# Performance work log

Hardware: AMD Instinct MI355X
Metric: run time of the kernel (lower is better)

The kernel has to match this reference:

```python
import jax, jax.numpy as jnp
import numpy as np

DIM = 1024
NUM_HEADS = 16
HEAD_DIM = DIM // NUM_HEADS


def apply_rope(x):
    # x: [B, S, H, D]
    seq_len = x.shape[1]
    inv_freq = 1.0 / (10000.0 ** (jnp.arange(0, HEAD_DIM, 2, dtype=jnp.float32) / HEAD_DIM))
    t = jnp.arange(seq_len, dtype=jnp.float32)
    freqs = jnp.outer(t, inv_freq)                      # [S, D/2]
    emb = jnp.concatenate([freqs, freqs], axis=-1)      # [S, D]
    cos = jnp.cos(emb)[None, :, None, :]                # [1, S, 1, D]
    sin = jnp.sin(emb)[None, :, None, :]
    x1, x2 = jnp.split(x, 2, axis=-1)
    x_rot = jnp.concatenate([-x2, x1], axis=-1)
    return x * cos + x_rot * sin


def setup_inputs() -> dict:
    key = jax.random.key(0)
    kx, kq, kk, kv, ko = jax.random.split(key, 5)
    scale = 1.0 / np.sqrt(DIM)
    return {
        "x": jax.random.normal(kx, (2, 2048, DIM), dtype=jnp.float32),
        "Wq": jax.random.normal(kq, (DIM, DIM), dtype=jnp.float32) * scale,
        "Wk": jax.random.normal(kk, (DIM, DIM), dtype=jnp.float32) * scale,
        "Wv": jax.random.normal(kv, (DIM, DIM), dtype=jnp.float32) * scale,
        "Wo": jax.random.normal(ko, (DIM, DIM), dtype=jnp.float32) * scale,
    }


def reference(x, Wq, Wk, Wv, Wo):
    B, S, _ = x.shape
    # torch nn.Linear: y = x @ W.T
    q = (x @ Wq.T).reshape(B, S, NUM_HEADS, HEAD_DIM)
    k = (x @ Wk.T).reshape(B, S, NUM_HEADS, HEAD_DIM)
    v = (x @ Wv.T).reshape(B, S, NUM_HEADS, HEAD_DIM)
    q = apply_rope(q)
    k = apply_rope(k)
    # attention over [B, H, S, D]; non-causal, no dropout (eval mode)
    scale = 1.0 / np.sqrt(HEAD_DIM)
    scores = jnp.einsum("bqhd,bkhd->bhqk", q, k) * scale
    attn = jax.nn.softmax(scores, axis=-1)
    out = jnp.einsum("bhqk,bkhd->bqhd", attn, v).reshape(B, S, DIM)
    return out @ Wo.T
```

## Files before the change

### kernel.cpp

```cpp
#include <hip/hip_runtime.h>

#define DIM   1024
#define NHEAD 16
#define HD    64
#define SEQ   2048
#define BATCH 2
#define MROWS (BATCH * SEQ)
#define NT    (SEQ / 64)

typedef __attribute__((ext_vector_type(8))) _Float16 s8h;
typedef __attribute__((ext_vector_type(4))) _Float16 s4h;
typedef __attribute__((ext_vector_type(4))) float f32x4;

typedef const __attribute__((address_space(1))) unsigned GU;
typedef __attribute__((address_space(3))) unsigned LU;

__device__ __forceinline__ void gll16(const void* g, void* l) {
    __builtin_amdgcn_global_load_lds((GU*)g, (LU*)l, 16, 0, 0);
}
__device__ __forceinline__ f32x4 mfma16(s8h a, s8h b, f32x4 c) {
    return __builtin_amdgcn_mfma_f32_16x16x32_f16(a, b, c, 0, 0, 0);
}
__device__ __forceinline__ float ex2(float x) {
    return __builtin_amdgcn_exp2f(x);
}

__global__ __launch_bounds__(256) void cast_f16_kernel(
    const float* __restrict__ x,  const float* __restrict__ wq,
    const float* __restrict__ wk, const float* __restrict__ wv,
    const float* __restrict__ wo,
    _Float16* __restrict__ xh,  _Float16* __restrict__ wqh,
    _Float16* __restrict__ wkh, _Float16* __restrict__ wvh,
    _Float16* __restrict__ woh) {
    int id = blockIdx.x * 256 + threadIdx.x;
    const float* src; _Float16* dst; size_t off;
    if (id < 524288) { src = x; dst = xh; off = (size_t)id * 8; }
    else {
        int r = id - 524288, w = r >> 17, o = r & 131071;
        src = (w == 0) ? wq : (w == 1) ? wk : (w == 2) ? wv : wo;
        dst = (w == 0) ? wqh : (w == 1) ? wkh : (w == 2) ? wvh : woh;
        off = (size_t)o * 8;
    }
    float4 v0 = *(const float4*)(src + off);
    float4 v1 = *(const float4*)(src + off + 4);
    s8h y;
    y[0]=(_Float16)v0.x; y[1]=(_Float16)v0.y; y[2]=(_Float16)v0.z; y[3]=(_Float16)v0.w;
    y[4]=(_Float16)v1.x; y[5]=(_Float16)v1.y; y[6]=(_Float16)v1.z; y[7]=(_Float16)v1.w;
    *(s8h*)(dst + off) = y;
}

__global__ __launch_bounds__(256) void rope_table_kernel(float2* __restrict__ tbl) {
    int idx = blockIdx.x * 256 + threadIdx.x;
    int s = idx >> 5, i = idx & 31;
    float freq = powf(10000.0f, -(float)(2 * i) * (1.0f / 64.0f));
    float ang  = (float)s * freq;
    tbl[idx] = make_float2(cosf(ang), sinf(ang));
}

template <bool F32OUT>
__device__ __forceinline__ void gemm_core(const _Float16* __restrict__ A,
                                          const _Float16* __restrict__ Bw,
                                          void* __restrict__ C, int ldc,
                                          int rowBase, int colBase) {
    __shared__ _Float16 As[128][64];
    __shared__ _Float16 Bs[128][64];
    const int tid = threadIdx.x, wid = tid >> 6, l = tid & 63;
    const int g = l >> 4, li = l & 15;
    const int wr = wid >> 1, wc = wid & 1;

    f32x4 acc[4][4];
#pragma unroll
    for (int m = 0; m < 4; ++m)
#pragma unroll
        for (int n = 0; n < 4; ++n) acc[m][n] = (f32x4){0.f, 0.f, 0.f, 0.f};

    const int srow = l >> 3;
    const int schunk = l & 7;

    for (int kt = 0; kt < DIM / 64; ++kt) {
#pragma unroll
        for (int i = 0; i < 4; ++i) {
            int c = wid * 4 + i;
            gll16(A  + (size_t)(rowBase + c * 8 + srow) * DIM + kt * 64 + schunk * 8, &As[c * 8][0]);
            gll16(Bw + (size_t)(colBase + c * 8 + srow) * DIM + kt * 64 + schunk * 8, &Bs[c * 8][0]);
        }
        __syncthreads();
        s8h a[4][2], b[4][2];
#pragma unroll
        for (int m = 0; m < 4; ++m) {
            int row = wr * 64 + m * 16 + li;
            a[m][0] = *(const s8h*)&As[row][g * 8];
            a[m][1] = *(const s8h*)&As[row][32 + g * 8];
        }
#pragma unroll
        for (int n = 0; n < 4; ++n) {
            int col = wc * 64 + n * 16 + li;
            b[n][0] = *(const s8h*)&Bs[col][g * 8];
            b[n][1] = *(const s8h*)&Bs[col][32 + g * 8];
        }
#pragma unroll
        for (int m = 0; m < 4; ++m)
#pragma unroll
            for (int n = 0; n < 4; ++n) {
                acc[m][n] = mfma16(a[m][0], b[n][0], acc[m][n]);
                acc[m][n] = mfma16(a[m][1], b[n][1], acc[m][n]);
            }
        __syncthreads();
    }
#pragma unroll
    for (int m = 0; m < 4; ++m)
#pragma unroll
        for (int n = 0; n < 4; ++n)
#pragma unroll
            for (int j = 0; j < 4; ++j) {
                int r = rowBase + wr * 64 + m * 16 + g * 4 + j;
                int c = colBase + wc * 64 + n * 16 + li;
                if (F32OUT) ((float*)C)[(size_t)r * ldc + c] = acc[m][n][j];
                else        ((_Float16*)C)[(size_t)r * ldc + c] = (_Float16)acc[m][n][j];
            }
}

__global__ __launch_bounds__(256) void gemm_qkv_kernel(
    const _Float16* __restrict__ X,
    const _Float16* __restrict__ Wq, const _Float16* __restrict__ Wk,
    const _Float16* __restrict__ Wv,
    _Float16* __restrict__ Q, _Float16* __restrict__ K,
    _Float16* __restrict__ Vt) {
    if (blockIdx.z == 2) {
        gemm_core<false>(Wv, X, Vt, MROWS, blockIdx.x * 128, blockIdx.y * 128);
    } else {
        const _Float16* B = (blockIdx.z == 0) ? Wq : Wk;
        _Float16* C       = (blockIdx.z == 0) ? Q  : K;
        gemm_core<false>(X, B, C, DIM, blockIdx.y * 128, blockIdx.x * 128);
    }
}
__global__ __launch_bounds__(256) void gemm_out_kernel(
    const _Float16* __restrict__ AO, const _Float16* __restrict__ Wo,
    float* __restrict__ OUT) {
    gemm_core<true>(AO, Wo, OUT, DIM, blockIdx.y * 128, blockIdx.x * 128);
}

__global__ __launch_bounds__(256) void rope_f16_kernel(_Float16* __restrict__ Q,
                                                       _Float16* __restrict__ K,
                                                       const float2* __restrict__ tbl) {
    int id = blockIdx.x * 256 + threadIdx.x;
    int c = id & 3, h = (id >> 2) & 15, row = (id >> 6) & 4095;
    _Float16* X = (id >> 18) ? K : Q;
    int s = row & (SEQ - 1);
    size_t base = (size_t)row * DIM + h * HD + c * 8;
    s8h x1 = *(const s8h*)(X + base);
    s8h x2 = *(const s8h*)(X + base + 32);
    const float4* tp = (const float4*)(tbl + s * 32 + c * 8);
    float4 t0 = tp[0], t1 = tp[1], t2 = tp[2], t3 = tp[3];
    float cs[8] = {t0.x, t0.z, t1.x, t1.z, t2.x, t2.z, t3.x, t3.z};
    float sn[8] = {t0.y, t0.w, t1.y, t1.w, t2.y, t2.w, t3.y, t3.w};
    s8h y1, y2;
#pragma unroll
    for (int e = 0; e < 8; ++e) {
        float a = (float)x1[e], bq = (float)x2[e];
        y1[e] = (_Float16)fmaf(a, cs[e], -bq * sn[e]);
        y2[e] = (_Float16)fmaf(bq, cs[e],  a * sn[e]);
    }
    *(s8h*)(X + base)      = y1;
    *(s8h*)(X + base + 32) = y2;
}

__global__ __launch_bounds__(256, 2) void attn_kernel(const _Float16* __restrict__ Q,
                                                      const _Float16* __restrict__ K,
                                                      const _Float16* __restrict__ Vt,
                                                      _Float16* __restrict__ AO) {
    __shared__ _Float16 Ks[2][64][64];
    __shared__ _Float16 Vs[2][64][64];

    const int tid = threadIdx.x, wid = tid >> 6, l = tid & 63;
    const int g = l >> 4, li = l & 15;
    const int qt = blockIdx.x, h = blockIdx.y, b = blockIdx.z;

    const _Float16* Qh  = Q  + ((size_t)(b * SEQ) + qt * 128 + wid * 32) * DIM + h * HD;
    const _Float16* Kh  = K  + (size_t)(b * SEQ) * DIM + h * HD;
    const _Float16* Vth = Vt + (size_t)(h * HD) * MROWS + b * SEQ;
    _Float16* AOh = AO + ((size_t)(b * SEQ) + qt * 128 + wid * 32) * DIM + h * HD;

    const int srow   = l >> 3;
    const int schunk = (l & 7) ^ srow;
    const int p7 = li & 7;

    s8h qf[2][2];
#pragma unroll
    for (int nt = 0; nt < 2; ++nt)
#pragma unroll
        for (int dc = 0; dc < 2; ++dc)
            qf[nt][dc] = *(const s8h*)(Qh + (size_t)(nt * 16 + li) * DIM + dc * 32 + g * 8);

    f32x4 o[4][2];
    float mrun[2], lrun[2];
#pragma unroll
    for (int nt = 0; nt < 2; ++nt) { mrun[nt] = -INFINITY; lrun[nt] = 0.f; }
#pragma unroll
    for (int mtd = 0; mtd < 4; ++mtd)
#pragma unroll
        for (int nt = 0; nt < 2; ++nt) o[mtd][nt] = (f32x4){0.f, 0.f, 0.f, 0.f};

    const float C1 = 0.125f * 1.44269504088896f;

#pragma unroll
    for (int i = 0; i < 2; ++i) {
        int r = wid * 16 + i * 8;
        gll16(Kh  + (size_t)(r + srow) * DIM   + schunk * 8, &Ks[0][r][0]);
        gll16(Vth + (size_t)(r + srow) * MROWS + schunk * 8, &Vs[0][r][0]);
    }

    for (int kt = 0; kt < NT; ++kt) {
        const int buf = kt & 1;
        __syncthreads();

        if (kt + 1 < NT) {
#pragma unroll
            for (int i = 0; i < 2; ++i) {
                int r = wid * 16 + i * 8;
                gll16(Kh  + (size_t)((kt + 1) * 64 + r + srow) * DIM + schunk * 8,
                      &Ks[buf ^ 1][r][0]);
                gll16(Vth + (size_t)(r + srow) * MROWS + (kt + 1) * 64 + schunk * 8,
                      &Vs[buf ^ 1][r][0]);
            }
        }

        f32x4 st[4][2];
#pragma unroll
        for (int mt = 0; mt < 4; ++mt)
#pragma unroll
            for (int nt = 0; nt < 2; ++nt) st[mt][nt] = (f32x4){0.f, 0.f, 0.f, 0.f};
#pragma unroll
        for (int mt = 0; mt < 4; ++mt) {
            const _Float16* krow = &Ks[buf][mt * 16 + li][0];
            s8h k0 = *(const s8h*)(krow + ((0 + g) ^ p7) * 8);
            s8h k1 = *(const s8h*)(krow + ((4 + g) ^ p7) * 8);
#pragma unroll
            for (int nt = 0; nt < 2; ++nt) {
                st[mt][nt] = mfma16(k0, qf[nt][0], st[mt][nt]);
                st[mt][nt] = mfma16(k1, qf[nt][1], st[mt][nt]);
            }
        }

        s4h va[4][2][2];
#pragma unroll
        for (int mtd = 0; mtd < 4; ++mtd)
#pragma unroll
            for (int kc = 0; kc < 2; ++kc) {
                const _Float16* vrow = &Vs[buf][mtd * 16 + li][0];
                int c0 = kc * 4 + (g >> 1), ofs = (g & 1) * 4;
                va[mtd][kc][0] = *(const s4h*)(vrow + ((c0 + 0) ^ p7) * 8 + ofs);
                va[mtd][kc][1] = *(const s4h*)(vrow + ((c0 + 2) ^ p7) * 8 + ofs);
            }

#pragma unroll
        for (int nt = 0; nt < 2; ++nt) {
            float tm = st[0][nt][0];
#pragma unroll
            for (int mt = 0; mt < 4; ++mt)
#pragma unroll
                for (int jj = 0; jj < 4; ++jj)
                    if (mt || jj) tm = fmaxf(tm, st[mt][nt][jj]);
            tm = fmaxf(tm, __shfl_xor(tm, 16));
            tm = fmaxf(tm, __shfl_xor(tm, 32));
            float mo = mrun[nt];
            float mn = fmaxf(mo, tm);
            float alpha = ex2((mo - mn) * C1);
            float rs = 0.f;
#pragma unroll
            for (int mt = 0; mt < 4; ++mt)
#pragma unroll
                for (int jj = 0; jj < 4; ++jj) {
                    float p = ex2((st[mt][nt][jj] - mn) * C1);
                    st[mt][nt][jj] = p;
                    rs += p;
                }
            rs += __shfl_xor(rs, 16);
            rs += __shfl_xor(rs, 32);
            lrun[nt] = lrun[nt] * alpha + rs;
            mrun[nt] = mn;
#pragma unroll
            for (int mtd = 0; mtd < 4; ++mtd) {
                o[mtd][nt][0] *= alpha; o[mtd][nt][1] *= alpha;
                o[mtd][nt][2] *= alpha; o[mtd][nt][3] *= alpha;
            }
        }

        s8h pb[2][2];
#pragma unroll
        for (int nt = 0; nt < 2; ++nt)
#pragma unroll
            for (int kc = 0; kc < 2; ++kc)
#pragma unroll
                for (int e = 0; e < 8; ++e)
                    pb[nt][kc][e] = (_Float16)st[kc * 2 + (e >> 2)][nt][e & 3];

#pragma unroll
        for (int mtd = 0; mtd < 4; ++mtd)
#pragma unroll
            for (int kc = 0; kc < 2; ++kc) {
                s8h v8;
#pragma unroll
                for (int e = 0; e < 4; ++e) { v8[e] = va[mtd][kc][0][e]; v8[4 + e] = va[mtd][kc][1][e]; }
#pragma unroll
                for (int nt = 0; nt < 2; ++nt)
                    o[mtd][nt] = mfma16(v8, pb[nt][kc], o[mtd][nt]);
            }
    }

#pragma unroll
    for (int nt = 0; nt < 2; ++nt) {
        float inv = 1.0f / lrun[nt];
#pragma unroll
        for (int mtd = 0; mtd < 4; ++mtd) {
            s4h w;
#pragma unroll
            for (int jj = 0; jj < 4; ++jj) w[jj] = (_Float16)(o[mtd][nt][jj] * inv);
            *(s4h*)(AOh + (size_t)(nt * 16 + li) * DIM + mtd * 16 + g * 4) = w;
        }
    }
}

extern "C" void kernel_launch(void* const* d_in, const int* in_sizes, int n_in,
                              void* d_out, int out_size, void* d_ws, size_t ws_size,
                              hipStream_t stream) {
    const float* x  = (const float*)d_in[0];
    const float* Wq = (const float*)d_in[1];
    const float* Wk = (const float*)d_in[2];
    const float* Wv = (const float*)d_in[3];
    const float* Wo = (const float*)d_in[4];
    float* out = (float*)d_out;

    char* ws = (char*)d_ws;
    _Float16* xh  = (_Float16*)(ws);
    _Float16* Wqh = (_Float16*)(ws + 8388608);
    _Float16* Wkh = (_Float16*)(ws + 10485760);
    _Float16* Wvh = (_Float16*)(ws + 12582912);
    _Float16* Woh = (_Float16*)(ws + 14680064);
    _Float16* Qh  = (_Float16*)(ws + 16777216);
    _Float16* Kh  = (_Float16*)(ws + 25165824);
    _Float16* Vth = (_Float16*)(ws + 33554432);
    _Float16* AOh = (_Float16*)(ws + 41943040);
    float2*   tbl = (float2*)  (ws + 50331648);

    cast_f16_kernel<<<4096, 256, 0, stream>>>(x, Wq, Wk, Wv, Wo, xh, Wqh, Wkh, Wvh, Woh);
    rope_table_kernel<<<256, 256, 0, stream>>>(tbl);
    gemm_qkv_kernel<<<dim3(8, 32, 3), 256, 0, stream>>>(xh, Wqh, Wkh, Wvh, Qh, Kh, Vth);
    rope_f16_kernel<<<2048, 256, 0, stream>>>(Qh, Kh, tbl);
    attn_kernel<<<dim3(16, 16, 2), 256, 0, stream>>>(Qh, Kh, Vth, AOh);
    gemm_out_kernel<<<dim3(8, 32), 256, 0, stream>>>(AOh, Woh, out);
}
```

Measured before the change: 233.7 us.

## Fuse RoPE into QKV GEMM epilogue, merge prep kernels, swizzle blocks, lazy rescale

Merges the rope table build into the cast kernel and applies RoPE inside the Q/K GEMM epilogue in fp32, removing two launches and a read-modify-write pass over Q and K. Adds block-index swizzles to the GEMMs and the attention kernel to change which tiles run together for cache reuse. In attention, the softmax running max is only updated and the output rescaled when a wave-wide check finds the new max exceeds the old by a threshold, skipping most alpha rescales. The lazy rescale lets exponentials grow up to 2^8 before renormalising, which relies on fp16/fp32 headroom.

```diff
diff --git a/kernel.cpp b/kernel.cpp
--- a/kernel.cpp
+++ b/kernel.cpp
@@ -25,13 +25,21 @@
     return __builtin_amdgcn_exp2f(x);
 }
 
-__global__ __launch_bounds__(256) void cast_f16_kernel(
+__global__ __launch_bounds__(256) void prep_kernel(
     const float* __restrict__ x,  const float* __restrict__ wq,
     const float* __restrict__ wk, const float* __restrict__ wv,
     const float* __restrict__ wo,
     _Float16* __restrict__ xh,  _Float16* __restrict__ wqh,
     _Float16* __restrict__ wkh, _Float16* __restrict__ wvh,
-    _Float16* __restrict__ woh) {
+    _Float16* __restrict__ woh, float2* __restrict__ tbl) {
+    if (blockIdx.x >= 4096) {
+        int idx = (blockIdx.x - 4096) * 256 + threadIdx.x;
+        int s = idx >> 5, i = idx & 31;
+        float freq = powf(10000.0f, -(float)(2 * i) * (1.0f / 64.0f));
+        float ang  = (float)s * freq;
+        tbl[idx] = make_float2(cosf(ang), sinf(ang));
+        return;
+    }
     int id = blockIdx.x * 256 + threadIdx.x;
     const float* src; _Float16* dst; size_t off;
     if (id < 524288) { src = x; dst = xh; off = (size_t)id * 8; }
@@ -49,19 +57,12 @@
     *(s8h*)(dst + off) = y;
 }
 
-__global__ __launch_bounds__(256) void rope_table_kernel(float2* __restrict__ tbl) {
-    int idx = blockIdx.x * 256 + threadIdx.x;
-    int s = idx >> 5, i = idx & 31;
-    float freq = powf(10000.0f, -(float)(2 * i) * (1.0f / 64.0f));
-    float ang  = (float)s * freq;
-    tbl[idx] = make_float2(cosf(ang), sinf(ang));
-}
-
-template <bool F32OUT>
+template <bool F32OUT, bool ROPE>
 __device__ __forceinline__ void gemm_core(const _Float16* __restrict__ A,
                                           const _Float16* __restrict__ Bw,
                                           void* __restrict__ C, int ldc,
-                                          int rowBase, int colBase) {
+                                          int rowBase, int colBase,
+                                          const float2* __restrict__ tbl) {
     __shared__ _Float16 As[128][64];
     __shared__ _Float16 Bs[128][64];
     const int tid = threadIdx.x, wid = tid >> 6, l = tid & 63;
@@ -110,14 +111,25 @@
 #pragma unroll
     for (int m = 0; m < 4; ++m)
 #pragma unroll
-        for (int n = 0; n < 4; ++n)
-#pragma unroll
-            for (int j = 0; j < 4; ++j) {
-                int r = rowBase + wr * 64 + m * 16 + g * 4 + j;
+        for (int j = 0; j < 4; ++j) {
+            int r = rowBase + wr * 64 + m * 16 + g * 4 + j;
+            if (ROPE) {
+                int s = r & (SEQ - 1);
+#pragma unroll
+                for (int n = 0; n < 2; ++n) {
+                    float2 cs = tbl[s * 32 + n * 16 + li];
+                    float av = acc[m][n][j], bv = acc[m][n + 2][j];
+                    acc[m][n][j]     = av * cs.x - bv * cs.y;
+                    acc[m][n + 2][j] = bv * cs.x + av * cs.y;
+                }
+            }
+#pragma unroll
+            for (int n = 0; n < 4; ++n) {
                 int c = colBase + wc * 64 + n * 16 + li;
                 if (F32OUT) ((float*)C)[(size_t)r * ldc + c] = acc[m][n][j];
                 else        ((_Float16*)C)[(size_t)r * ldc + c] = (_Float16)acc[m][n][j];
             }
+        }
 }
 
 __global__ __launch_bounds__(256) void gemm_qkv_kernel(
@@ -125,44 +137,25 @@
     const _Float16* __restrict__ Wq, const _Float16* __restrict__ Wk,
     const _Float16* __restrict__ Wv,
     _Float16* __restrict__ Q, _Float16* __restrict__ K,
-    _Float16* __restrict__ Vt) {
-    if (blockIdx.z == 2) {
-        gemm_core<false>(Wv, X, Vt, MROWS, blockIdx.x * 128, blockIdx.y * 128);
+    _Float16* __restrict__ Vt, const float2* __restrict__ tbl) {
+    int lin = blockIdx.x + (blockIdx.y << 3) + (blockIdx.z << 8);
+    int swz = (lin & 7) * 96 + (lin >> 3);
+    int bx = swz & 7, by = (swz >> 3) & 31, bz = swz >> 8;
+    if (bz == 2) {
+        gemm_core<false, false>(Wv, X, Vt, MROWS, bx * 128, by * 128, nullptr);
+    } else if (bz == 0) {
+        gemm_core<false, true>(X, Wq, Q, DIM, by * 128, bx * 128, tbl);
     } else {
-        const _Float16* B = (blockIdx.z == 0) ? Wq : Wk;
-        _Float16* C       = (blockIdx.z == 0) ? Q  : K;
-        gemm_core<false>(X, B, C, DIM, blockIdx.y * 128, blockIdx.x * 128);
+        gemm_core<false, true>(X, Wk, K, DIM, by * 128, bx * 128, tbl);
     }
 }
 __global__ __launch_bounds__(256) void gemm_out_kernel(
     const _Float16* __restrict__ AO, const _Float16* __restrict__ Wo,
     float* __restrict__ OUT) {
-    gemm_core<true>(AO, Wo, OUT, DIM, blockIdx.y * 128, blockIdx.x * 128);
-}
-
-__global__ __launch_bounds__(256) void rope_f16_kernel(_Float16* __restrict__ Q,
-                                                       _Float16* __restrict__ K,
-                                                       const float2* __restrict__ tbl) {
-    int id = blockIdx.x * 256 + threadIdx.x;
-    int c = id & 3, h = (id >> 2) & 15, row = (id >> 6) & 4095;
-    _Float16* X = (id >> 18) ? K : Q;
-    int s = row & (SEQ - 1);
-    size_t base = (size_t)row * DIM + h * HD + c * 8;
-    s8h x1 = *(const s8h*)(X + base);
-    s8h x2 = *(const s8h*)(X + base + 32);
-    const float4* tp = (const float4*)(tbl + s * 32 + c * 8);
-    float4 t0 = tp[0], t1 = tp[1], t2 = tp[2], t3 = tp[3];
-    float cs[8] = {t0.x, t0.z, t1.x, t1.z, t2.x, t2.z, t3.x, t3.z};
-    float sn[8] = {t0.y, t0.w, t1.y, t1.w, t2.y, t2.w, t3.y, t3.w};
-    s8h y1, y2;
-#pragma unroll
-    for (int e = 0; e < 8; ++e) {
-        float a = (float)x1[e], bq = (float)x2[e];
-        y1[e] = (_Float16)fmaf(a, cs[e], -bq * sn[e]);
-        y2[e] = (_Float16)fmaf(bq, cs[e],  a * sn[e]);
-    }
-    *(s8h*)(X + base)      = y1;
-    *(s8h*)(X + base + 32) = y2;
+    int lin = blockIdx.x + (blockIdx.y << 3);
+    int swz = (lin & 7) * 32 + (lin >> 3);
+    int bx = swz & 7, by = swz >> 3;
+    gemm_core<true, false>(AO, Wo, OUT, DIM, by * 128, bx * 128, nullptr);
 }
 
 __global__ __launch_bounds__(256, 2) void attn_kernel(const _Float16* __restrict__ Q,
@@ -174,7 +167,9 @@
 
     const int tid = threadIdx.x, wid = tid >> 6, l = tid & 63;
     const int g = l >> 4, li = l & 15;
-    const int qt = blockIdx.x, h = blockIdx.y, b = blockIdx.z;
+    int lin = blockIdx.x + (blockIdx.y << 4) + (blockIdx.z << 8);
+    int swz = (lin & 7) * 64 + (lin >> 3);
+    const int qt = swz & 15, h = (swz >> 4) & 15, b = swz >> 8;
 
     const _Float16* Qh  = Q  + ((size_t)(b * SEQ) + qt * 128 + wid * 32) * DIM + h * HD;
     const _Float16* Kh  = K  + (size_t)(b * SEQ) * DIM + h * HD;
@@ -202,6 +197,7 @@
         for (int nt = 0; nt < 2; ++nt) o[mtd][nt] = (f32x4){0.f, 0.f, 0.f, 0.f};
 
     const float C1 = 0.125f * 1.44269504088896f;
+    const float DTHR = 8.0f / C1;
 
 #pragma unroll
     for (int i = 0; i < 2; ++i) {
@@ -255,35 +251,38 @@
 
 #pragma unroll
         for (int nt = 0; nt < 2; ++nt) {
-            float tm = st[0][nt][0];
-#pragma unroll
-            for (int mt = 0; mt < 4; ++mt)
-#pragma unroll
-                for (int jj = 0; jj < 4; ++jj)
-                    if (mt || jj) tm = fmaxf(tm, st[mt][nt][jj]);
+            float t0 = fmaxf(fmaxf(st[0][nt][0], st[0][nt][1]), fmaxf(st[0][nt][2], st[0][nt][3]));
+            float t1 = fmaxf(fmaxf(st[1][nt][0], st[1][nt][1]), fmaxf(st[1][nt][2], st[1][nt][3]));
+            float t2 = fmaxf(fmaxf(st[2][nt][0], st[2][nt][1]), fmaxf(st[2][nt][2], st[2][nt][3]));
+            float t3 = fmaxf(fmaxf(st[3][nt][0], st[3][nt][1]), fmaxf(st[3][nt][2], st[3][nt][3]));
+            float tm = fmaxf(fmaxf(t0, t1), fmaxf(t2, t3));
             tm = fmaxf(tm, __shfl_xor(tm, 16));
             tm = fmaxf(tm, __shfl_xor(tm, 32));
             float mo = mrun[nt];
-            float mn = fmaxf(mo, tm);
-            float alpha = ex2((mo - mn) * C1);
+            if (!__all(tm <= mo + DTHR)) {
+                float mn = fmaxf(mo, tm);
+                float alpha = ex2((mo - mn) * C1);
+                lrun[nt] *= alpha;
+                mrun[nt] = mn;
+#pragma unroll
+                for (int mtd = 0; mtd < 4; ++mtd) {
+                    o[mtd][nt][0] *= alpha; o[mtd][nt][1] *= alpha;
+                    o[mtd][nt][2] *= alpha; o[mtd][nt][3] *= alpha;
+                }
+            }
+            float mnow = mrun[nt];
             float rs = 0.f;
 #pragma unroll
             for (int mt = 0; mt < 4; ++mt)
 #pragma unroll
                 for (int jj = 0; jj < 4; ++jj) {
-                    float p = ex2((st[mt][nt][jj] - mn) * C1);
+                    float p = ex2((st[mt][nt][jj] - mnow) * C1);
                     st[mt][nt][jj] = p;
                     rs += p;
                 }
             rs += __shfl_xor(rs, 16);
             rs += __shfl_xor(rs, 32);
-            lrun[nt] = lrun[nt] * alpha + rs;
-            mrun[nt] = mn;
-#pragma unroll
-            for (int mtd = 0; mtd < 4; ++mtd) {
-                o[mtd][nt][0] *= alpha; o[mtd][nt][1] *= alpha;
-                o[mtd][nt][2] *= alpha; o[mtd][nt][3] *= alpha;
-            }
+            lrun[nt] += rs;
         }
 
         s8h pb[2][2];
@@ -343,10 +342,8 @@
     _Float16* AOh = (_Float16*)(ws + 41943040);
     float2*   tbl = (float2*)  (ws + 50331648);
 
-    cast_f16_kernel<<<4096, 256, 0, stream>>>(x, Wq, Wk, Wv, Wo, xh, Wqh, Wkh, Wvh, Woh);
-    rope_table_kernel<<<256, 256, 0, stream>>>(tbl);
-    gemm_qkv_kernel<<<dim3(8, 32, 3), 256, 0, stream>>>(xh, Wqh, Wkh, Wvh, Qh, Kh, Vth);
-    rope_f16_kernel<<<2048, 256, 0, stream>>>(Qh, Kh, tbl);
+    prep_kernel<<<4352, 256, 0, stream>>>(x, Wq, Wk, Wv, Wo, xh, Wqh, Wkh, Wvh, Woh, tbl);
+    gemm_qkv_kernel<<<dim3(8, 32, 3), 256, 0, stream>>>(xh, Wqh, Wkh, Wvh, Qh, Kh, Vth, tbl);
     attn_kernel<<<dim3(16, 16, 2), 256, 0, stream>>>(Qh, Kh, Vth, AOh);
     gemm_out_kernel<<<dim3(8, 32), 256, 0, stream>>>(AOh, Woh, out);
 }
```

Measured after the change: 222.4 us. 4.8% less time.
